# Kernel optimization log

Measured on AMD Instinct MI355X. Metric: run time of the kernel, lower is better.

Reference implementation:

```python
import jax, jax.numpy as jnp
import numpy as np

L = 40   # seq_length (sentence includes root; sent_length = L-1)
B = 16   # batch
V = 10000  # vocab
F = 512  # feature_size = 2*hidden (bidirectional)
H = 256  # classifier hidden
NEG = -jnp.inf


def _mlp(x, W1, b1, W2, b2):
    # Classifier / BinaryClassifier: Linear -> tanh -> Linear
    return jnp.tanh(x @ W1 + b1) @ W2 + b2


def setup_inputs() -> dict:
    key = jax.random.key(0)
    ks = jax.random.split(key, 10)
    s = 0.05
    return {
        "h": jax.random.normal(ks[0], (L, B, F), jnp.float32),
        "sentence": jax.random.randint(ks[1], (L, B), 0, V),
        "Wt1": jax.random.normal(ks[2], (2 * F, H), jnp.float32) * s,
        "bt1": jnp.zeros((H,), jnp.float32),
        "Wt2": jax.random.normal(ks[3], (H, 1), jnp.float32) * s,
        "bt2": jnp.zeros((1,), jnp.float32),
        "Ww1": jax.random.normal(ks[4], (2 * F, H), jnp.float32) * s,
        "bw1": jnp.zeros((H,), jnp.float32),
        "Ww2": jax.random.normal(ks[5], (H, V), jnp.float32) * s,
        "bw2": jnp.zeros((V,), jnp.float32),
    }


def reference(h, sentence, Wt1, bt1, Wt2, bt2, Ww1, bw1, Ww2, bw2):
    sent_length = L - 1
    # all ordered pairs i < j (forward enumeration order of batch_feature_selection)
    iu, ju = np.triu_indices(L, k=1)          # [P]
    feat = jnp.concatenate([h[iu], h[ju]], axis=-1)   # [P, B, 2F]

    t_logit = _mlp(feat, Wt1, bt1, Wt2, bt2)[..., 0]  # [P, B]
    sh = jax.nn.log_sigmoid(-t_logit)                 # shift log-prob
    re = jax.nn.log_sigmoid(t_logit)                  # reduce log-prob

    # word model log-softmax, gathered at target token sentence[j+1]
    wl = _mlp(feat, Ww1, bw1, Ww2, bw2)               # [P, B, V]
    ju1 = np.minimum(ju + 1, L - 1)                   # pairs with j = L-1 are unused
    tgt = sentence[ju1]                               # [P, B]
    gathered = jnp.take_along_axis(wl, tgt[..., None], axis=-1)[..., 0]
    wlp = gathered - jax.nn.logsumexp(wl, axis=-1)    # [P, B]

    # dense [L, L, B] tables (only i<j entries used)
    SHW = jnp.full((L, L, B), NEG, jnp.float32).at[iu, ju].set(sh + wlp)  # word_prob_list
    RE = jnp.full((L, L, B), NEG, jnp.float32).at[iu, ju].set(re)

    # init cell: stack_next=False -> word prob of sentence[1] from features (0,0)
    feat0 = jnp.concatenate([h[0], h[0]], axis=-1)    # [B, 2F]
    lp0 = jax.nn.log_softmax(_mlp(feat0, Ww1, bw1, Ww2, bw2), axis=-1)
    init = jnp.take_along_axis(lp0, sentence[1][:, None], axis=1)[:, 0]  # [B]

    T = jnp.full((L, L, B), NEG, jnp.float32)
    T = T.at[0, 1].set(init)
    T = T.at[jnp.arange(1, sent_length), jnp.arange(2, sent_length + 1)].set(0.0)

    # CKY-style DP over span widths; each width is vectorized over start i and split k
    for gap in range(2, sent_length + 1):
        n_i = sent_length + 1 - gap
        i_arr = np.arange(n_i)
        j_arr = i_arr + gap
        k = i_arr[:, None] + np.arange(1, gap)[None, :]   # [n_i, gap-1]
        scores = (T[i_arr[:, None], k] + T[k, j_arr[:, None]]
                  + SHW[i_arr[:, None], k] + RE[k, j_arr[:, None]])  # [n_i, gap-1, B]
        T = T.at[i_arr, j_arr].set(jax.nn.logsumexp(scores, axis=1))

    # stack_next=False -> final_score = 0
    return T[0, sent_length]
```

## Files before the change

### kernel.cpp

```cpp
#include <hip/hip_runtime.h>
#include <hip/hip_bf16.h>

#define L_SEQ 40
#define B_SZ  16
#define V_SZ  10000
#define V_PAD 10240
#define NPAIR 780
#define NROWP 784
#define M_ROWS (NROWP * B_SZ)

typedef __attribute__((ext_vector_type(4))) float f32x4;
typedef __attribute__((ext_vector_type(4))) int   i32x4;
typedef __attribute__((ext_vector_type(8))) int   i32x8;

#if __has_builtin(__builtin_amdgcn_cvt_pk_fp8_f32)
__device__ __forceinline__ unsigned int pack4_fp8(float x0, float x1, float x2, float x3) {
    int lo = __builtin_amdgcn_cvt_pk_fp8_f32(x0, x1, 0, false);
    int full = __builtin_amdgcn_cvt_pk_fp8_f32(x2, x3, lo, true);
    return (unsigned int)full;
}
#else
__device__ __forceinline__ unsigned char f2e4m3(float f) {
    unsigned u = __float_as_uint(f);
    unsigned s = (u >> 24) & 0x80u;
    if ((u & 0x7FFFFFFFu) == 0) return (unsigned char)s;
    int E = (int)((u >> 23) & 0xFF) - 127 + 7;
    unsigned m = u & 0x7FFFFFu;
    if (E >= 16) return (unsigned char)(s | 0x7E);
    if (E >= 1) {
        unsigned keep = m >> 20, rest = m & 0xFFFFFu;
        keep += (rest > 0x80000u) || (rest == 0x80000u && (keep & 1));
        if (keep == 8) { keep = 0; E++; if (E >= 16) return (unsigned char)(s | 0x7E); }
        return (unsigned char)(s | (E << 3) | keep);
    }
    int shift = 1 - E;
    if (shift > 10) return (unsigned char)s;
    unsigned full = 0x800000u | m;
    unsigned sh = 20 + shift;
    unsigned keep = full >> sh, rem = full & ((1u << sh) - 1), half = 1u << (sh - 1);
    keep += (rem > half) || (rem == half && (keep & 1));
    if (keep >= 8) return (unsigned char)(s | (1 << 3));
    return (unsigned char)(s | keep);
}
__device__ __forceinline__ unsigned int pack4_fp8(float x0, float x1, float x2, float x3) {
    return (unsigned int)f2e4m3(x0) | ((unsigned int)f2e4m3(x1) << 8)
         | ((unsigned int)f2e4m3(x2) << 16) | ((unsigned int)f2e4m3(x3) << 24);
}
#endif

#if __has_builtin(__builtin_amdgcn_exp2f)
__device__ __forceinline__ float exp2_hw(float x) { return __builtin_amdgcn_exp2f(x); }
#else
__device__ __forceinline__ float exp2_hw(float x) { return __expf(x * 0.6931471805599453f); }
#endif


__global__ __launch_bounds__(256) void prep_kernel(
        const float* __restrict__ Ww2, float* __restrict__ WwT,
        unsigned char* __restrict__ WbT,
        const float* __restrict__ h, const float* __restrict__ Wt1,
        const float* __restrict__ Ww1, float* __restrict__ UV,
        float* __restrict__ rowsum) {
    const int bx = blockIdx.x;
    const int t = threadIdx.x;
    __shared__ float tile[32][33];
    __shared__ float hs[8 * 512];
    if (bx < 2560) {
        int v0 = (bx % 320) * 32;
        int K8 = bx / 320;
        int k0 = K8 * 32;
        int tx = t & 31, ty = t >> 5;
#pragma unroll
        for (int r = 0; r < 4; r++) {
            int k = k0 + ty + r * 8;
            int v = v0 + tx;
            tile[ty + r * 8][tx] = (v < V_SZ) ? Ww2[k * V_SZ + v] : 0.0f;
        }
        __syncthreads();
#pragma unroll
        for (int r = 0; r < 4; r++) {
            int vrow = ty + r * 8;
            WwT[(v0 + vrow) * 256 + (k0 + tx)] = tile[tx][vrow];
        }
        int v2 = t >> 3;
        int kq = 4 * (t & 7);
        unsigned int pk = pack4_fp8(tile[kq][v2], tile[kq + 1][v2],
                                    tile[kq + 2][v2], tile[kq + 3][v2]);
        ((unsigned int*)WbT)[(v0 + v2) * 64 + K8 * 8 + (t & 7)] = pk;
    } else if (bx < 2880) {
        int ub = bx - 2560;
        int which = ub / 80;
        int m0 = (ub % 80) * 8;
        const float4* src = (const float4*)(h + (size_t)m0 * 512);
        float4* dst4 = (float4*)hs;
#pragma unroll
        for (int v = 0; v < 4; v++) dst4[v * 256 + t] = src[v * 256 + t];
        __syncthreads();
        const float* W = ((which < 2) ? Wt1 : Ww1) + ((which & 1) ? 512 * 256 : 0);
        float acc[8] = {};
        for (int f = 0; f < 512; f += 4) {
            float w0 = W[(f + 0) * 256 + t];
            float w1 = W[(f + 1) * 256 + t];
            float w2 = W[(f + 2) * 256 + t];
            float w3 = W[(f + 3) * 256 + t];
#pragma unroll
            for (int r = 0; r < 8; r++) {
                acc[r] += hs[r * 512 + f] * w0 + hs[r * 512 + f + 1] * w1
                        + hs[r * 512 + f + 2] * w2 + hs[r * 512 + f + 3] * w3;
            }
        }
        float* dst = UV + ((size_t)which * 640 + m0) * 256;
#pragma unroll
        for (int r = 0; r < 8; r++) dst[r * 256 + t] = acc[r];
    } else {
        int idx = (bx - 2880) * 256 + t;
        if (idx < M_ROWS) rowsum[idx] = 0.0f;
    }
}

__global__ void build_rows(const float* __restrict__ UV,
                           const int* __restrict__ sentence,
                           const float* __restrict__ bt1,
                           const float* __restrict__ bw1,
                           const float* __restrict__ Wt2,
                           const float* __restrict__ bt2,
                           const float* __restrict__ WwT,
                           const float* __restrict__ bw2,
                           unsigned char* __restrict__ X,
                           float* __restrict__ tlog,
                           float* __restrict__ glog) {
    int w = blockIdx.x * 4 + (threadIdx.x >> 6);
    int lane = threadIdx.x & 63;
    int p = w >> 4, b = w & 15;
    int i = 0, j = 0;
    if (p < NPAIR) {
        int rem = p, len = L_SEQ - 1;
        while (rem >= len) { rem -= len; len--; i++; }
        j = i + 1 + rem;
    }
    int j1 = (j + 1 < L_SEQ) ? j + 1 : L_SEQ - 1;
    int tgt = sentence[j1 * B_SZ + b];
    const float4 ut = ((const float4*)(UV + 0 * 640 * 256 + (i * B_SZ + b) * 256))[lane];
    const float4 vt = ((const float4*)(UV + 1 * 640 * 256 + (j * B_SZ + b) * 256))[lane];
    const float4 uw = ((const float4*)(UV + 2 * 640 * 256 + (i * B_SZ + b) * 256))[lane];
    const float4 vw = ((const float4*)(UV + 3 * 640 * 256 + (j * B_SZ + b) * 256))[lane];
    const float4 bt = ((const float4*)bt1)[lane];
    const float4 bw = ((const float4*)bw1)[lane];
    const float4 w2 = ((const float4*)Wt2)[lane];
    const float4 wc = ((const float4*)(WwT + (size_t)tgt * 256))[lane];
    float xt0 = tanhf(ut.x + vt.x + bt.x), xt1 = tanhf(ut.y + vt.y + bt.y);
    float xt2 = tanhf(ut.z + vt.z + bt.z), xt3 = tanhf(ut.w + vt.w + bt.w);
    float xw0 = tanhf(uw.x + vw.x + bw.x), xw1 = tanhf(uw.y + vw.y + bw.y);
    float xw2 = tanhf(uw.z + vw.z + bw.z), xw3 = tanhf(uw.w + vw.w + bw.w);
    ((unsigned int*)X)[w * 64 + lane] = pack4_fp8(xw0, xw1, xw2, xw3);
    float td = xt0 * w2.x + xt1 * w2.y + xt2 * w2.z + xt3 * w2.w;
    float gd = xw0 * wc.x + xw1 * wc.y + xw2 * wc.z + xw3 * wc.w;
#pragma unroll
    for (int off = 32; off >= 1; off >>= 1) {
        td += __shfl_xor(td, off);
        gd += __shfl_xor(gd, off);
    }
    if (lane == 0) {
        tlog[w] = td + bt2[0];
        glog[w] = gd + bw2[tgt];
    }
}

__global__ __launch_bounds__(256, 4) void big_gemm(
        const unsigned char* __restrict__ X,
        const unsigned char* __restrict__ WbT,
        const float* __restrict__ bw2,
        float* __restrict__ rowsum) {
    __shared__ unsigned char Bs[2][64 * 256];
    const int t = threadIdx.x;
    const int wid = t >> 6, lane = t & 63;
    const int l15 = lane & 15, l4 = lane >> 4;
    const int g = blockIdx.x;
    const int row0 = blockIdx.y * 128 + wid * 32;

    auto dmaB = [&](int buf, int it) {
        const unsigned char* Bg = WbT + (size_t)(g * 1024 + it * 64) * 256;
#pragma unroll
        for (int q = 0; q < 4; q++) {
            int base = (wid * 4 + q) * 1024;
            int F = base + lane * 16;
            int cc = F >> 8;
            int s = (F >> 4) & 15;
            int srcg = s ^ (cc & 15);
            __builtin_amdgcn_global_load_lds(
                (const __attribute__((address_space(1))) unsigned int*)(Bg + cc * 256 + (srcg << 4)),
                (__attribute__((address_space(3))) unsigned int*)(&Bs[buf][0] + base),
                16, 0, 0);
        }
    };

    dmaB(0, 0);

    i32x8 apan[2][2];
    {
        const unsigned char* Ag = X + (size_t)row0 * 256;
#pragma unroll
        for (int mi = 0; mi < 2; mi++)
#pragma unroll
            for (int kb = 0; kb < 2; kb++)
                apan[mi][kb] = *(const i32x8*)(Ag + (mi * 16 + l15) * 256 + kb * 128 + l4 * 32);
    }
    __syncthreads();

    float PS[2][4] = {};
    const float L2E = 1.44269504088896340736f;

#pragma unroll 1
    for (int it = 0; it < 16; it++) {
        if (it < 15) dmaB((it + 1) & 1, it + 1);
        const unsigned char* Bb = &Bs[it & 1][0];
        f32x4 acc[2][4] = {};
#pragma unroll
        for (int kb = 0; kb < 2; kb++) {
#pragma unroll
            for (int ni = 0; ni < 4; ni++) {
                int cc = ni * 16 + l15;
                int g0 = kb * 8 + l4 * 2;
                i32x4 lo = *(const i32x4*)(Bb + cc * 256 + (((g0 + 0) ^ (cc & 15)) << 4));
                i32x4 hi = *(const i32x4*)(Bb + cc * 256 + (((g0 + 1) ^ (cc & 15)) << 4));
                i32x8 bv = {lo.x, lo.y, lo.z, lo.w, hi.x, hi.y, hi.z, hi.w};
                acc[0][ni] = __builtin_amdgcn_mfma_scale_f32_16x16x128_f8f6f4(
                    apan[0][kb], bv, acc[0][ni], 0, 0,
                    0, 0x7F7F7F7F, 0, 0x7F7F7F7F);
                acc[1][ni] = __builtin_amdgcn_mfma_scale_f32_16x16x128_f8f6f4(
                    apan[1][kb], bv, acc[1][ni], 0, 0,
                    0, 0x7F7F7F7F, 0, 0x7F7F7F7F);
            }
        }
#pragma unroll
        for (int ni = 0; ni < 4; ni++) {
            int col = g * 1024 + it * 64 + ni * 16 + l15;
            float bL = (col < V_SZ) ? bw2[col] * L2E : -__builtin_inff();
#pragma unroll
            for (int mi = 0; mi < 2; mi++)
#pragma unroll
                for (int r = 0; r < 4; r++)
                    PS[mi][r] += exp2_hw(fmaf(acc[mi][ni][r], L2E, bL));
        }
        __syncthreads();
    }
#pragma unroll
    for (int mi = 0; mi < 2; mi++)
#pragma unroll
        for (int r = 0; r < 4; r++) {
            float v = PS[mi][r];
            v += __shfl_xor(v, 1); v += __shfl_xor(v, 2);
            v += __shfl_xor(v, 4); v += __shfl_xor(v, 8);
            if (l15 == 0)
                atomicAdd(&rowsum[row0 + mi * 16 + l4 * 4 + r], v);
        }
}

__global__ __launch_bounds__(1024) void dp_kernel(const float* __restrict__ tlog,
                          const float* __restrict__ glog,
                          const float* __restrict__ rowsum,
                          float* __restrict__ out) {
    __shared__ float Tl[1600], SHWl[1600], REl[1600];
    const int t = threadIdx.x;
    const int b = blockIdx.x;
    const float NEGINF = -__builtin_inff();
    for (int idx = t; idx < 1600; idx += 1024) {
        Tl[idx] = NEGINF; SHWl[idx] = NEGINF; REl[idx] = NEGINF;
    }
    __syncthreads();
    for (int p = t; p < NPAIR; p += 1024) {
        int i = 0, rem = p, len = L_SEQ - 1;
        while (rem >= len) { rem -= len; len--; i++; }
        int j = i + 1 + rem;
        int row = p * 16 + b;
        float tl = tlog[row];
        float re_v = (tl >= 0.f) ? -log1pf(__expf(-tl)) : (tl - log1pf(__expf(tl)));
        float sh_v = (tl <= 0.f) ? -log1pf(__expf(tl)) : (-tl - log1pf(__expf(-tl)));
        float wlp = glog[row] - __logf(rowsum[row]);
        SHWl[i * 40 + j] = sh_v + wlp;
        REl[i * 40 + j] = re_v;
    }
    if (t == 0) {
        int row = NPAIR * 16 + b;
        Tl[0 * 40 + 1] = glog[row] - __logf(rowsum[row]);
    }
    if (t >= 1 && t <= 38) Tl[t * 40 + t + 1] = 0.f;
    __syncthreads();
    const int tg = t >> 4, li = t & 15;
    for (int gap = 2; gap <= L_SEQ - 1; gap++) {
        int n_i = L_SEQ - gap;
        float m = NEGINF, s = 0.f;
        int i = tg, j = tg + gap;
        if (tg < n_i) {
            for (int k = i + 1 + li; k < j; k += 16) {
                float v = Tl[i * 40 + k] + Tl[k * 40 + j]
                        + SHWl[i * 40 + k] + REl[k * 40 + j];
                if (v > m) { s = s * __expf(m - v) + 1.f; m = v; }
                else s += __expf(v - m);
            }
        }
#pragma unroll
        for (int off = 1; off < 16; off <<= 1) {
            float mo = __shfl_xor(m, off), so = __shfl_xor(s, off);
            float M = fmaxf(m, mo);
            float sn = 0.f;
            if (m > NEGINF) sn += s * __expf(m - M);
            if (mo > NEGINF) sn += so * __expf(mo - M);
            m = M; s = sn;
        }
        if (tg < n_i && li == 0) Tl[i * 40 + j] = m + __logf(s);
        __syncthreads();
    }
    if (t == 0) out[b] = Tl[39];
}

extern "C" void kernel_launch(void* const* d_in, const int* in_sizes, int n_in,
                              void* d_out, int out_size, void* d_ws, size_t ws_size,
                              hipStream_t stream) {
    const float* h        = (const float*)d_in[0];
    const int*   sentence = (const int*)d_in[1];
    const float* Wt1      = (const float*)d_in[2];
    const float* bt1      = (const float*)d_in[3];
    const float* Wt2      = (const float*)d_in[4];
    const float* bt2      = (const float*)d_in[5];
    const float* Ww1      = (const float*)d_in[6];
    const float* bw1      = (const float*)d_in[7];
    const float* Ww2      = (const float*)d_in[8];
    const float* bw2      = (const float*)d_in[9];
    float* out = (float*)d_out;

    char* ws = (char*)d_ws;
    size_t off = 0;
    float* UV = (float*)(ws + off);                    off += 4ull * 640 * 256 * 4;
    unsigned char* X = (unsigned char*)(ws + off);     off += (size_t)M_ROWS * 256;
    unsigned char* WbT = (unsigned char*)(ws + off);   off += (size_t)V_PAD * 256;
    float* WwT = (float*)(ws + off);                   off += (size_t)V_PAD * 256 * 4;
    float* rowsum = (float*)(ws + off);                off += (size_t)M_ROWS * 4;
    float* tlog = (float*)(ws + off);                  off += (size_t)M_ROWS * 4;
    float* glog = (float*)(ws + off);                  off += (size_t)M_ROWS * 4;

    const int zero_blocks = (M_ROWS + 255) / 256;
    prep_kernel<<<2880 + zero_blocks, 256, 0, stream>>>(
        Ww2, WwT, WbT, h, Wt1, Ww1, UV, rowsum);
    build_rows<<<M_ROWS / 4, 256, 0, stream>>>(UV, sentence, bt1, bw1, Wt2, bt2,
                                               WwT, bw2, X, tlog, glog);
    big_gemm<<<dim3(10, 98), 256, 0, stream>>>(X, WbT, bw2, rowsum);
    dp_kernel<<<16, 1024, 0, stream>>>(tlog, glog, rowsum, out);
}
```

Before: 217.7 us.

## Triple-buffer GEMM B tiles with one barrier per step and fast tanh

```diff
diff --git a/kernel.cpp b/kernel.cpp
--- a/kernel.cpp
+++ b/kernel.cpp
@@ -53,6 +53,17 @@
 #else
 __device__ __forceinline__ float exp2_hw(float x) { return __expf(x * 0.6931471805599453f); }
 #endif
+
+#if __has_builtin(__builtin_amdgcn_rcpf)
+__device__ __forceinline__ float rcp_hw(float x) { return __builtin_amdgcn_rcpf(x); }
+#else
+__device__ __forceinline__ float rcp_hw(float x) { return 1.0f / x; }
+#endif
+
+__device__ __forceinline__ float fast_tanh(float x) {
+    float e = exp2_hw(x * 2.885390081777926814f);
+    return fmaf(-2.0f, rcp_hw(e + 1.0f), 1.0f);
+}
 
 
 __global__ __launch_bounds__(256) void prep_kernel(
@@ -148,10 +159,10 @@
     const float4 bw = ((const float4*)bw1)[lane];
     const float4 w2 = ((const float4*)Wt2)[lane];
     const float4 wc = ((const float4*)(WwT + (size_t)tgt * 256))[lane];
-    float xt0 = tanhf(ut.x + vt.x + bt.x), xt1 = tanhf(ut.y + vt.y + bt.y);
-    float xt2 = tanhf(ut.z + vt.z + bt.z), xt3 = tanhf(ut.w + vt.w + bt.w);
-    float xw0 = tanhf(uw.x + vw.x + bw.x), xw1 = tanhf(uw.y + vw.y + bw.y);
-    float xw2 = tanhf(uw.z + vw.z + bw.z), xw3 = tanhf(uw.w + vw.w + bw.w);
+    float xt0 = fast_tanh(ut.x + vt.x + bt.x), xt1 = fast_tanh(ut.y + vt.y + bt.y);
+    float xt2 = fast_tanh(ut.z + vt.z + bt.z), xt3 = fast_tanh(ut.w + vt.w + bt.w);
+    float xw0 = fast_tanh(uw.x + vw.x + bw.x), xw1 = fast_tanh(uw.y + vw.y + bw.y);
+    float xw2 = fast_tanh(uw.z + vw.z + bw.z), xw3 = fast_tanh(uw.w + vw.w + bw.w);
     ((unsigned int*)X)[w * 64 + lane] = pack4_fp8(xw0, xw1, xw2, xw3);
     float td = xt0 * w2.x + xt1 * w2.y + xt2 * w2.z + xt3 * w2.w;
     float gd = xw0 * wc.x + xw1 * wc.y + xw2 * wc.z + xw3 * wc.w;
@@ -166,35 +177,34 @@
     }
 }
 
-__global__ __launch_bounds__(256, 4) void big_gemm(
+__global__ __launch_bounds__(256, 3) void big_gemm(
         const unsigned char* __restrict__ X,
         const unsigned char* __restrict__ WbT,
         const float* __restrict__ bw2,
         float* __restrict__ rowsum) {
-    __shared__ unsigned char Bs[2][64 * 256];
+    __shared__ unsigned char Bs[3][64 * 256];
     const int t = threadIdx.x;
     const int wid = t >> 6, lane = t & 63;
     const int l15 = lane & 15, l4 = lane >> 4;
     const int g = blockIdx.x;
     const int row0 = blockIdx.y * 128 + wid * 32;
+    const int NIT = 20;
 
     auto dmaB = [&](int buf, int it) {
-        const unsigned char* Bg = WbT + (size_t)(g * 1024 + it * 64) * 256;
+        const unsigned char* Bg = WbT + (size_t)(g * 1280 + it * 64) * 256;
 #pragma unroll
         for (int q = 0; q < 4; q++) {
-            int base = (wid * 4 + q) * 1024;
-            int F = base + lane * 16;
+            int off = (wid * 4 + q) * 1024;
+            int F = off + lane * 16;
             int cc = F >> 8;
             int s = (F >> 4) & 15;
             int srcg = s ^ (cc & 15);
             __builtin_amdgcn_global_load_lds(
                 (const __attribute__((address_space(1))) unsigned int*)(Bg + cc * 256 + (srcg << 4)),
-                (__attribute__((address_space(3))) unsigned int*)(&Bs[buf][0] + base),
+                (__attribute__((address_space(3))) unsigned int*)(&Bs[buf][0] + off),
                 16, 0, 0);
         }
     };
-
-    dmaB(0, 0);
 
     i32x8 apan[2][2];
     {
@@ -205,15 +215,22 @@
             for (int kb = 0; kb < 2; kb++)
                 apan[mi][kb] = *(const i32x8*)(Ag + (mi * 16 + l15) * 256 + kb * 128 + l4 * 32);
     }
-    __syncthreads();
+    dmaB(0, 0);
+    dmaB(1, 1);
 
     float PS[2][4] = {};
     const float L2E = 1.44269504088896340736f;
+    int cur = 0, pre = 2;
 
 #pragma unroll 1
-    for (int it = 0; it < 16; it++) {
-        if (it < 15) dmaB((it + 1) & 1, it + 1);
-        const unsigned char* Bb = &Bs[it & 1][0];
+    for (int it = 0; it < NIT; it++) {
+        if (it < NIT - 1) {
+            asm volatile("s_waitcnt vmcnt(4)\n\ts_barrier" ::: "memory");
+        } else {
+            asm volatile("s_waitcnt vmcnt(0)\n\ts_barrier" ::: "memory");
+        }
+        if (it + 2 < NIT) dmaB(pre, it + 2);
+        const unsigned char* Bb = &Bs[cur][0];
         f32x4 acc[2][4] = {};
 #pragma unroll
         for (int kb = 0; kb < 2; kb++) {
@@ -234,7 +251,7 @@
         }
 #pragma unroll
         for (int ni = 0; ni < 4; ni++) {
-            int col = g * 1024 + it * 64 + ni * 16 + l15;
+            int col = g * 1280 + it * 64 + ni * 16 + l15;
             float bL = (col < V_SZ) ? bw2[col] * L2E : -__builtin_inff();
 #pragma unroll
             for (int mi = 0; mi < 2; mi++)
@@ -242,7 +259,8 @@
                 for (int r = 0; r < 4; r++)
                     PS[mi][r] += exp2_hw(fmaf(acc[mi][ni][r], L2E, bL));
         }
-        __syncthreads();
+        cur = (cur == 2) ? 0 : cur + 1;
+        pre = (pre == 2) ? 0 : pre + 1;
     }
 #pragma unroll
     for (int mi = 0; mi < 2; mi++)
@@ -344,6 +362,6 @@
         Ww2, WwT, WbT, h, Wt1, Ww1, UV, rowsum);
     build_rows<<<M_ROWS / 4, 256, 0, stream>>>(UV, sentence, bt1, bw1, Wt2, bt2,
                                                WwT, bw2, X, tlog, glog);
-    big_gemm<<<dim3(10, 98), 256, 0, stream>>>(X, WbT, bw2, rowsum);
+    big_gemm<<<dim3(8, 98), 256, 0, stream>>>(X, WbT, bw2, rowsum);
     dp_kernel<<<16, 1024, 0, stream>>>(tlog, glog, rowsum, out);
 }
```

Result: no change. 217.3 us (-0.2%).
